# Kernel tuning notes

Hardware: AMD Instinct MI355X
Metric: run time of the kernel (lower is better)

## Reference

```python
import jax, jax.numpy as jnp
import numpy as np

D_DEC = 256  # decoder_size; W columns are [decoder | encoder] per the torch concat order


def setup_inputs() -> dict:
    key = jax.random.key(0)
    k1, k2, k3, k4 = jax.random.split(key, 4)
    B, S, E, D, A = 32, 4096, 256, 256, 256
    decoder_hidden = jax.random.normal(k1, (1, B, D), dtype=jnp.float32)
    encoder_outputs = jax.random.normal(k2, (S, B, E), dtype=jnp.float32)
    W = jax.random.normal(k3, (A, D + E), dtype=jnp.float32) / np.sqrt(D + E)
    b = jax.random.normal(k4, (A,), dtype=jnp.float32) * 0.02
    return {"decoder_hidden": decoder_hidden, "encoder_outputs": encoder_outputs, "W": W, "b": b}


def reference(decoder_hidden, encoder_outputs, W, b):
    # decoder_hidden: [1,B,D] -> [B,D]; encoder_outputs: [S,B,E] -> [B,S,E]
    dh = decoder_hidden[0]
    eo = jnp.transpose(encoder_outputs, (1, 0, 2))
    # Split the concat-linear: cat([dec, enc]) @ W.T == dec @ Wd.T + enc @ We.T
    Wd, We = W[:, :D_DEC], W[:, D_DEC:]
    # scores: tanh(linear) summed over attn dim -> [B,S]
    proj = dh @ Wd.T + b  # [B,A]
    attn = jnp.tanh(proj[:, None, :] + jnp.einsum('bse,ae->bsa', eo, We))
    scores = jnp.sum(attn, axis=2)  # [B,S]
    attn_softmax = jax.nn.softmax(scores, axis=1)  # [B,S]
    attended = jnp.einsum('bs,bse->be', attn_softmax, eo)  # [B,E]
    encoder_norms = jnp.linalg.norm(eo, axis=2)  # [B,S]
    attn_map = attn_softmax * encoder_norms
    return attended, attn_map
```

## Files before the change

### kernel.cpp

```cpp
#include <hip/hip_runtime.h>
#include <math.h>

#define B_  32
#define S_  4096
#define E_  256
#define A_  256
#define DE_ 512

typedef __attribute__((ext_vector_type(8))) short short8;
typedef __attribute__((ext_vector_type(4))) float f32x4;

__device__ inline unsigned short f2bf(float x) {
    unsigned int u = __float_as_uint(x);
    u += 0x7FFFu + ((u >> 16) & 1u);
    return (unsigned short)(u >> 16);
}
__device__ inline float tanh_fast(float x) {
    x = fminf(fmaxf(x, -15.f), 15.f);
    float t = __expf(2.f * x);
    return (t - 1.f) * __builtin_amdgcn_rcpf(t + 1.f);
}

__global__ __launch_bounds__(256) void prep_kernel(
    const float* __restrict__ W, const float* __restrict__ dh,
    const float* __restrict__ bias, unsigned short* __restrict__ wepk,
    float* __restrict__ proj, float* __restrict__ out)
{
    __shared__ float dh_lds[E_];
    const int bk  = blockIdx.x;
    const int tid = threadIdx.x;
    if (bk < 64) {
        const int idx = bk * 256 + tid;
        const int c     = idx >> 11;
        const int r     = idx & 2047;
        const int plane = r >> 10;
        const int kg    = (r >> 8) & 3;
        const int a     = r & 255;
        const float* src = W + (size_t)a * DE_ + E_ + c * 32 + kg * 8;
        unsigned int pk[4];
        #pragma unroll
        for (int j = 0; j < 4; ++j) {
            float x0 = src[2 * j], x1 = src[2 * j + 1];
            unsigned int u0 = __float_as_uint(x0) & 0xFFFF0000u;
            unsigned int u1 = __float_as_uint(x1) & 0xFFFF0000u;
            if (plane) {
                unsigned short l0 = f2bf(x0 - __uint_as_float(u0));
                unsigned short l1 = f2bf(x1 - __uint_as_float(u1));
                pk[j] = (unsigned int)l0 | ((unsigned int)l1 << 16);
            } else {
                pk[j] = (u0 >> 16) | u1;
            }
        }
        *(uint4*)&wepk[(size_t)idx * 8] = make_uint4(pk[0], pk[1], pk[2], pk[3]);
    } else if (bk < 96) {
        const int b = bk - 64;
        const int a = tid;
        dh_lds[a] = dh[b * E_ + a];
        __syncthreads();
        float acc = bias[a];
        const float* wrow = W + (size_t)a * DE_;
        #pragma unroll
        for (int d = 0; d < E_; d += 4) {
            float4 w = *(const float4*)(wrow + d);
            acc += dh_lds[d] * w.x + dh_lds[d+1] * w.y
                 + dh_lds[d+2] * w.z + dh_lds[d+3] * w.w;
        }
        proj[b * A_ + a] = acc;
    } else {
        #pragma unroll
        for (int j = tid; j < B_ * E_; j += 256) out[j] = 0.f;
    }
}

__global__ __launch_bounds__(256, 3) void scores_kernel(
    const float* __restrict__ eo, const unsigned short* __restrict__ wepk,
    const float* __restrict__ proj,
    float* __restrict__ scores, float* __restrict__ nsq)
{
    __shared__ __align__(16) unsigned short eo_lds[2 * 528 * 8];
    __shared__ float red4[64 * 65];
    __shared__ float npart[512];
    __shared__ float qpart[256];

    const int tid = threadIdx.x;
    const int b   = blockIdx.x & (B_ - 1);
    const int s0  = (blockIdx.x / B_) * 64;
    const int w   = tid >> 6, l = tid & 63;
    const int lq  = l >> 4,  lr = l & 15;

    const int erow0 = tid >> 3;
    const int ekq   = tid & 7;
    const int ekg   = ekq >> 1, eh = ekq & 1;
    const float* ebase = eo + (size_t)(s0 + erow0) * (B_ * E_) + b * E_ + ekq * 4;

    const unsigned short* wb = wepk + (size_t)(lq * 256 + w * 64 + lr) * 8;

    f32x4 acc[4][4];
    #pragma unroll
    for (int i = 0; i < 4; ++i)
        #pragma unroll
        for (int j = 0; j < 4; ++j)
            acc[i][j] = (f32x4){0.f, 0.f, 0.f, 0.f};
    float nacc[2] = {0.f, 0.f};

    float4 ec0 = *(const float4*)(ebase);
    float4 ec1 = *(const float4*)(ebase + 32 * (B_ * E_));
    short8 bh[4], bl[4], bnh[4], bnl[4];
    #pragma unroll
    for (int nt = 0; nt < 4; ++nt) {
        bh[nt] = *(const short8*)(wb + (size_t)(nt * 16) * 8);
        bl[nt] = *(const short8*)(wb + (size_t)(1024 + nt * 16) * 8);
    }

    #pragma unroll
    for (int c = 0; c < 8; ++c) {
        const int wbuf = (c & 1) * 528;
        #pragma unroll
        for (int it = 0; it < 2; ++it) {
            float4 v = it ? ec1 : ec0;
            nacc[it] += v.x*v.x + v.y*v.y + v.z*v.z + v.w*v.w;
            unsigned int ux = __float_as_uint(v.x) & 0xFFFF0000u;
            unsigned int uy = __float_as_uint(v.y) & 0xFFFF0000u;
            unsigned int uz = __float_as_uint(v.z) & 0xFFFF0000u;
            unsigned int uw = __float_as_uint(v.w) & 0xFFFF0000u;
            unsigned int hp0 = (ux >> 16) | uy;
            unsigned int hp1 = (uz >> 16) | uw;
            unsigned int lp0 = (unsigned int)f2bf(v.x - __uint_as_float(ux))
                             | ((unsigned int)f2bf(v.y - __uint_as_float(uy)) << 16);
            unsigned int lp1 = (unsigned int)f2bf(v.z - __uint_as_float(uz))
                             | ((unsigned int)f2bf(v.w - __uint_as_float(uw)) << 16);
            const int u = wbuf + ekg * 66 + it * 32 + erow0;
            *(uint2*)&eo_lds[(size_t)u * 8 + eh * 4]         = make_uint2(hp0, hp1);
            *(uint2*)&eo_lds[(size_t)(u + 264) * 8 + eh * 4] = make_uint2(lp0, lp1);
        }
        __syncthreads();
        if (c < 7) {
            ec0 = *(const float4*)(ebase + (c + 1) * 32);
            ec1 = *(const float4*)(ebase + 32 * (B_ * E_) + (c + 1) * 32);
            #pragma unroll
            for (int nt = 0; nt < 4; ++nt) {
                bnh[nt] = *(const short8*)(wb + (size_t)((c+1)*2048 + nt*16) * 8);
                bnl[nt] = *(const short8*)(wb + (size_t)((c+1)*2048 + 1024 + nt*16) * 8);
            }
        }
        #pragma unroll
        for (int mt = 0; mt < 4; ++mt) {
            const int au = wbuf + lq * 66 + mt * 16 + lr;
            short8 ah = *(const short8*)&eo_lds[(size_t)au * 8];
            short8 al = *(const short8*)&eo_lds[(size_t)(au + 264) * 8];
            #pragma unroll
            for (int nt = 0; nt < 4; ++nt) {
                acc[mt][nt] = __builtin_amdgcn_mfma_f32_16x16x32_bf16(ah, bh[nt], acc[mt][nt], 0, 0, 0);
                acc[mt][nt] = __builtin_amdgcn_mfma_f32_16x16x32_bf16(ah, bl[nt], acc[mt][nt], 0, 0, 0);
                acc[mt][nt] = __builtin_amdgcn_mfma_f32_16x16x32_bf16(al, bh[nt], acc[mt][nt], 0, 0, 0);
            }
        }
        if (c < 7) {
            #pragma unroll
            for (int nt = 0; nt < 4; ++nt) { bh[nt] = bnh[nt]; bl[nt] = bnl[nt]; }
        }
    }

    float pr[4];
    #pragma unroll
    for (int nt = 0; nt < 4; ++nt) pr[nt] = proj[b * A_ + w * 64 + nt * 16 + lr];
    #pragma unroll
    for (int mt = 0; mt < 4; ++mt) {
        #pragma unroll
        for (int r = 0; r < 4; ++r) {
            float s = 0.f;
            #pragma unroll
            for (int nt = 0; nt < 4; ++nt)
                s += tanh_fast(pr[nt] + acc[mt][nt][r]);
            red4[(w * 16 + lr) * 65 + (mt * 16 + lq * 4 + r)] = s;
        }
    }
    npart[tid]       = nacc[0];
    npart[256 + tid] = nacc[1];
    __syncthreads();
    {
        const int r = tid & 63, q = tid >> 6;
        float s = 0.f;
        #pragma unroll
        for (int c2 = q * 16; c2 < q * 16 + 16; ++c2) s += red4[c2 * 65 + r];
        qpart[q * 64 + r] = s;
    }
    __syncthreads();
    if (tid < 64) {
        scores[b * S_ + s0 + tid] = qpart[tid] + qpart[64 + tid]
                                  + qpart[128 + tid] + qpart[192 + tid];
        const int base = (tid >> 5) * 256 + (tid & 31) * 8;
        float nq = 0.f;
        #pragma unroll
        for (int q2 = 0; q2 < 8; ++q2) nq += npart[base + q2];
        nsq[b * S_ + s0 + tid] = nq;
    }
}

__global__ __launch_bounds__(256) void attend_kernel(
    const float* __restrict__ eo, const float* __restrict__ scores,
    const float* __restrict__ nsq, float* __restrict__ out)
{
    __shared__ float red[256];
    __shared__ float4 acc_red[4][64];
    const int tid = threadIdx.x;
    const int b   = blockIdx.x & (B_ - 1);
    const int ch  = blockIdx.x / B_;

    float v[16];
    float m = -1e30f;
    #pragma unroll
    for (int i = 0; i < 16; ++i) {
        v[i] = scores[b * S_ + i * 256 + tid];
        m = fmaxf(m, v[i]);
    }
    red[tid] = m;
    __syncthreads();
    for (int off = 128; off > 0; off >>= 1) {
        if (tid < off) red[tid] = fmaxf(red[tid], red[tid + off]);
        __syncthreads();
    }
    m = red[0];
    __syncthreads();
    float sum = 0.f;
    #pragma unroll
    for (int i = 0; i < 16; ++i) sum += __expf(v[i] - m);
    red[tid] = sum;
    __syncthreads();
    for (int off = 128; off > 0; off >>= 1) {
        if (tid < off) red[tid] += red[tid + off];
        __syncthreads();
    }
    const float inv = 1.f / red[0];

    const int le = tid & 63, sg = tid >> 6;
    const int s0 = ch * 128 + sg * 32;
    float4 a = make_float4(0.f, 0.f, 0.f, 0.f);
    #pragma unroll 4
    for (int s = 0; s < 32; ++s) {
        float pv = __expf(scores[b * S_ + s0 + s] - m) * inv;
        float4 e = *(const float4*)(eo + (size_t)(s0 + s) * (B_ * E_)
                                       + b * E_ + le * 4);
        a.x = fmaf(pv, e.x, a.x);
        a.y = fmaf(pv, e.y, a.y);
        a.z = fmaf(pv, e.z, a.z);
        a.w = fmaf(pv, e.w, a.w);
    }
    acc_red[sg][le] = a;
    if (tid < 128) {
        const int s = ch * 128 + tid;
        float pv = __expf(scores[b * S_ + s] - m) * inv;
        out[B_ * E_ + b * S_ + s] = pv * sqrtf(nsq[b * S_ + s]);
    }
    __syncthreads();
    if (tid < 64) {
        float4 a0 = acc_red[0][tid], a1 = acc_red[1][tid];
        float4 a2 = acc_red[2][tid], a3 = acc_red[3][tid];
        float* dst = out + b * E_ + tid * 4;
        atomicAdd(dst + 0, a0.x + a1.x + a2.x + a3.x);
        atomicAdd(dst + 1, a0.y + a1.y + a2.y + a3.y);
        atomicAdd(dst + 2, a0.z + a1.z + a2.z + a3.z);
        atomicAdd(dst + 3, a0.w + a1.w + a2.w + a3.w);
    }
}

extern "C" void kernel_launch(void* const* d_in, const int* in_sizes, int n_in,
                              void* d_out, int out_size, void* d_ws, size_t ws_size,
                              hipStream_t stream)
{
    const float* dh   = (const float*)d_in[0];
    const float* eo   = (const float*)d_in[1];
    const float* W    = (const float*)d_in[2];
    const float* bias = (const float*)d_in[3];
    float* out = (float*)d_out;
    float* ws  = (float*)d_ws;

    float* projb  = ws;
    float* nsqb   = ws + 8192;
    float* scores = nsqb + S_ * B_;
    unsigned short* wepk = (unsigned short*)(scores + S_ * B_);

    prep_kernel   <<<97,              256, 0, stream>>>(W, dh, bias, wepk, projb, out);
    scores_kernel <<<B_ * (S_ / 64),  256, 0, stream>>>(eo, wepk, projb, scores, nsqb);
    attend_kernel <<<B_ * (S_ / 128), 256, 0, stream>>>(eo, scores, nsqb, out);
}
```

Baseline: 273.2 us.

## Double scores tile to 128 rows and stage We in LDS via global_load_lds

```diff
diff --git a/kernel.cpp b/kernel.cpp
--- a/kernel.cpp
+++ b/kernel.cpp
@@ -72,82 +72,88 @@
     }
 }
 
-__global__ __launch_bounds__(256, 3) void scores_kernel(
+__global__ __launch_bounds__(256, 2) void scores_kernel(
     const float* __restrict__ eo, const unsigned short* __restrict__ wepk,
     const float* __restrict__ proj,
     float* __restrict__ scores, float* __restrict__ nsq)
 {
-    __shared__ __align__(16) unsigned short eo_lds[2 * 528 * 8];
-    __shared__ float red4[64 * 65];
-    __shared__ float npart[512];
-    __shared__ float qpart[256];
+    __shared__ __align__(16) unsigned char pool[49408];
+    unsigned short* we_hl = (unsigned short*)pool;
+    unsigned short* eo_hl = (unsigned short*)(pool + 32768);
 
     const int tid = threadIdx.x;
     const int b   = blockIdx.x & (B_ - 1);
-    const int s0  = (blockIdx.x / B_) * 64;
+    const int s0  = (blockIdx.x >> 5) * 128;
     const int w   = tid >> 6, l = tid & 63;
     const int lq  = l >> 4,  lr = l & 15;
 
-    const int erow0 = tid >> 3;
-    const int ekq   = tid & 7;
-    const int ekg   = ekq >> 1, eh = ekq & 1;
-    const float* ebase = eo + (size_t)(s0 + erow0) * (B_ * E_) + b * E_ + ekq * 4;
-
-    const unsigned short* wb = wepk + (size_t)(lq * 256 + w * 64 + lr) * 8;
-
-    f32x4 acc[4][4];
-    #pragma unroll
-    for (int i = 0; i < 4; ++i)
+    const int erow = tid >> 2;
+    const int ekg  = tid & 3;
+    const float* ebase = eo + (size_t)(s0 + erow) * (B_ * E_) + b * E_ + ekg * 8;
+
+    f32x4 acc[8][4];
+    #pragma unroll
+    for (int i = 0; i < 8; ++i)
         #pragma unroll
         for (int j = 0; j < 4; ++j)
             acc[i][j] = (f32x4){0.f, 0.f, 0.f, 0.f};
     float nacc[2] = {0.f, 0.f};
 
-    float4 ec0 = *(const float4*)(ebase);
-    float4 ec1 = *(const float4*)(ebase + 32 * (B_ * E_));
-    short8 bh[4], bl[4], bnh[4], bnl[4];
-    #pragma unroll
-    for (int nt = 0; nt < 4; ++nt) {
-        bh[nt] = *(const short8*)(wb + (size_t)(nt * 16) * 8);
-        bl[nt] = *(const short8*)(wb + (size_t)(1024 + nt * 16) * 8);
-    }
-
-    #pragma unroll
+    float4 ea0 = *(const float4*)(ebase);
+    float4 ea1 = *(const float4*)(ebase + 4);
+    float4 eb0 = *(const float4*)(ebase + (size_t)64 * (B_ * E_));
+    float4 eb1 = *(const float4*)(ebase + (size_t)64 * (B_ * E_) + 4);
+
     for (int c = 0; c < 8; ++c) {
-        const int wbuf = (c & 1) * 528;
+        __syncthreads();
         #pragma unroll
         for (int it = 0; it < 2; ++it) {
-            float4 v = it ? ec1 : ec0;
-            nacc[it] += v.x*v.x + v.y*v.y + v.z*v.z + v.w*v.w;
-            unsigned int ux = __float_as_uint(v.x) & 0xFFFF0000u;
-            unsigned int uy = __float_as_uint(v.y) & 0xFFFF0000u;
-            unsigned int uz = __float_as_uint(v.z) & 0xFFFF0000u;
-            unsigned int uw = __float_as_uint(v.w) & 0xFFFF0000u;
-            unsigned int hp0 = (ux >> 16) | uy;
-            unsigned int hp1 = (uz >> 16) | uw;
-            unsigned int lp0 = (unsigned int)f2bf(v.x - __uint_as_float(ux))
-                             | ((unsigned int)f2bf(v.y - __uint_as_float(uy)) << 16);
-            unsigned int lp1 = (unsigned int)f2bf(v.z - __uint_as_float(uz))
-                             | ((unsigned int)f2bf(v.w - __uint_as_float(uw)) << 16);
-            const int u = wbuf + ekg * 66 + it * 32 + erow0;
-            *(uint2*)&eo_lds[(size_t)u * 8 + eh * 4]         = make_uint2(hp0, hp1);
-            *(uint2*)&eo_lds[(size_t)(u + 264) * 8 + eh * 4] = make_uint2(lp0, lp1);
+            float4 v0 = it ? eb0 : ea0;
+            float4 v1 = it ? eb1 : ea1;
+            nacc[it] += v0.x*v0.x + v0.y*v0.y + v0.z*v0.z + v0.w*v0.w
+                      + v1.x*v1.x + v1.y*v1.y + v1.z*v1.z + v1.w*v1.w;
+            float xs[8] = {v0.x, v0.y, v0.z, v0.w, v1.x, v1.y, v1.z, v1.w};
+            unsigned int hp[4], lp[4];
+            #pragma unroll
+            for (int j = 0; j < 4; ++j) {
+                unsigned int u0 = __float_as_uint(xs[2*j])   & 0xFFFF0000u;
+                unsigned int u1 = __float_as_uint(xs[2*j+1]) & 0xFFFF0000u;
+                hp[j] = (u0 >> 16) | u1;
+                lp[j] = (unsigned int)f2bf(xs[2*j]   - __uint_as_float(u0))
+                      | ((unsigned int)f2bf(xs[2*j+1] - __uint_as_float(u1)) << 16);
+            }
+            const int u = ekg * 130 + it * 64 + erow;
+            *(uint4*)&eo_hl[(size_t)u * 8]         = make_uint4(hp[0], hp[1], hp[2], hp[3]);
+            *(uint4*)&eo_hl[(size_t)(520 + u) * 8] = make_uint4(lp[0], lp[1], lp[2], lp[3]);
+        }
+        const unsigned short* gsrc = wepk + (size_t)c * 2048 * 8;
+        #pragma unroll
+        for (int it = 0; it < 8; ++it) {
+            const int u = it * 256 + tid;
+            __builtin_amdgcn_global_load_lds(
+                (const __attribute__((address_space(1))) void*)(gsrc + (size_t)u * 8),
+                (__attribute__((address_space(3))) void*)&we_hl[(size_t)u * 8],
+                16, 0, 0);
         }
         __syncthreads();
         if (c < 7) {
-            ec0 = *(const float4*)(ebase + (c + 1) * 32);
-            ec1 = *(const float4*)(ebase + 32 * (B_ * E_) + (c + 1) * 32);
-            #pragma unroll
-            for (int nt = 0; nt < 4; ++nt) {
-                bnh[nt] = *(const short8*)(wb + (size_t)((c+1)*2048 + nt*16) * 8);
-                bnl[nt] = *(const short8*)(wb + (size_t)((c+1)*2048 + 1024 + nt*16) * 8);
-            }
-        }
-        #pragma unroll
-        for (int mt = 0; mt < 4; ++mt) {
-            const int au = wbuf + lq * 66 + mt * 16 + lr;
-            short8 ah = *(const short8*)&eo_lds[(size_t)au * 8];
-            short8 al = *(const short8*)&eo_lds[(size_t)(au + 264) * 8];
+            ea0 = *(const float4*)(ebase + (c + 1) * 32);
+            ea1 = *(const float4*)(ebase + (c + 1) * 32 + 4);
+            eb0 = *(const float4*)(ebase + (size_t)64 * (B_ * E_) + (c + 1) * 32);
+            eb1 = *(const float4*)(ebase + (size_t)64 * (B_ * E_) + (c + 1) * 32 + 4);
+        }
+        short8 bh[4], bl[4];
+        #pragma unroll
+        for (int nt = 0; nt < 4; ++nt) {
+            const int bunit = lq * 256 + w * 64 + nt * 16 + lr;
+            bh[nt] = *(const short8*)&we_hl[(size_t)bunit * 8];
+            bl[nt] = *(const short8*)&we_hl[(size_t)(1024 + bunit) * 8];
+        }
+        #pragma unroll
+        for (int mt = 0; mt < 8; ++mt) {
+            const int au = lq * 130 + mt * 16 + lr;
+            short8 ah = *(const short8*)&eo_hl[(size_t)au * 8];
+            short8 al = *(const short8*)&eo_hl[(size_t)(520 + au) * 8];
             #pragma unroll
             for (int nt = 0; nt < 4; ++nt) {
                 acc[mt][nt] = __builtin_amdgcn_mfma_f32_16x16x32_bf16(ah, bh[nt], acc[mt][nt], 0, 0, 0);
@@ -155,45 +161,42 @@
                 acc[mt][nt] = __builtin_amdgcn_mfma_f32_16x16x32_bf16(al, bh[nt], acc[mt][nt], 0, 0, 0);
             }
         }
-        if (c < 7) {
-            #pragma unroll
-            for (int nt = 0; nt < 4; ++nt) { bh[nt] = bnh[nt]; bl[nt] = bnl[nt]; }
-        }
-    }
-
+    }
+    __syncthreads();
+
+    float* red4  = (float*)pool;
+    float* npart = (float*)(pool + 33280);
+    float* qpart = (float*)(pool + 35328);
     float pr[4];
     #pragma unroll
     for (int nt = 0; nt < 4; ++nt) pr[nt] = proj[b * A_ + w * 64 + nt * 16 + lr];
     #pragma unroll
-    for (int mt = 0; mt < 4; ++mt) {
+    for (int mt = 0; mt < 8; ++mt) {
         #pragma unroll
         for (int r = 0; r < 4; ++r) {
             float s = 0.f;
             #pragma unroll
             for (int nt = 0; nt < 4; ++nt)
                 s += tanh_fast(pr[nt] + acc[mt][nt][r]);
-            red4[(w * 16 + lr) * 65 + (mt * 16 + lq * 4 + r)] = s;
+            red4[(w * 16 + lr) * 130 + (mt * 16 + lq * 4 + r)] = s;
         }
     }
     npart[tid]       = nacc[0];
     npart[256 + tid] = nacc[1];
     __syncthreads();
     {
-        const int r = tid & 63, q = tid >> 6;
+        const int row = tid >> 1, half = tid & 1;
         float s = 0.f;
         #pragma unroll
-        for (int c2 = q * 16; c2 < q * 16 + 16; ++c2) s += red4[c2 * 65 + r];
-        qpart[q * 64 + r] = s;
-    }
-    __syncthreads();
-    if (tid < 64) {
-        scores[b * S_ + s0 + tid] = qpart[tid] + qpart[64 + tid]
-                                  + qpart[128 + tid] + qpart[192 + tid];
-        const int base = (tid >> 5) * 256 + (tid & 31) * 8;
-        float nq = 0.f;
-        #pragma unroll
-        for (int q2 = 0; q2 < 8; ++q2) nq += npart[base + q2];
-        nsq[b * S_ + s0 + tid] = nq;
+        for (int j = 0; j < 32; ++j) s += red4[(half * 32 + j) * 130 + row];
+        qpart[half * 128 + row] = s;
+    }
+    __syncthreads();
+    if (tid < 128) {
+        scores[b * S_ + s0 + tid] = qpart[tid] + qpart[128 + tid];
+        const int base = (tid < 64) ? 4 * tid : 256 + 4 * (tid - 64);
+        nsq[b * S_ + s0 + tid] = npart[base] + npart[base + 1]
+                               + npart[base + 2] + npart[base + 3];
     }
 }
 
@@ -236,7 +239,7 @@
     const int le = tid & 63, sg = tid >> 6;
     const int s0 = ch * 128 + sg * 32;
     float4 a = make_float4(0.f, 0.f, 0.f, 0.f);
-    #pragma unroll 4
+    #pragma unroll 8
     for (int s = 0; s < 32; ++s) {
         float pv = __expf(scores[b * S_ + s0 + s] - m) * inv;
         float4 e = *(const float4*)(eo + (size_t)(s0 + s) * (B_ * E_)
@@ -281,6 +284,6 @@
     unsigned short* wepk = (unsigned short*)(scores + S_ * B_);
 
     prep_kernel   <<<97,              256, 0, stream>>>(W, dh, bias, wepk, projb, out);
-    scores_kernel <<<B_ * (S_ / 64),  256, 0, stream>>>(eo, wepk, projb, scores, nsqb);
+    scores_kernel <<<B_ * (S_ / 128), 256, 0, stream>>>(eo, wepk, projb, scores, nsqb);
     attend_kernel <<<B_ * (S_ / 128), 256, 0, stream>>>(eo, scores, nsqb, out);
 }
```

New measurement: 259.4 us. -5.1%, faster.

## Switch scores GEMM to 32x32x16 MFMA with LDS-staged weights via global_load_lds

Applied to the files above, without the earlier changes.

```diff
diff --git a/kernel.cpp b/kernel.cpp
--- a/kernel.cpp
+++ b/kernel.cpp
@@ -7,8 +7,8 @@
 #define A_  256
 #define DE_ 512
 
-typedef __attribute__((ext_vector_type(8))) short short8;
-typedef __attribute__((ext_vector_type(4))) float f32x4;
+typedef __attribute__((ext_vector_type(8)))  short short8;
+typedef __attribute__((ext_vector_type(16))) float f32x16;
 
 __device__ inline unsigned short f2bf(float x) {
     unsigned int u = __float_as_uint(x);
@@ -30,13 +30,13 @@
     const int bk  = blockIdx.x;
     const int tid = threadIdx.x;
     if (bk < 64) {
-        const int idx = bk * 256 + tid;
-        const int c     = idx >> 11;
-        const int r     = idx & 2047;
-        const int plane = r >> 10;
-        const int kg    = (r >> 8) & 3;
+        const int idx   = bk * 256 + tid;
+        const int c     = idx >> 10;
+        const int r     = idx & 1023;
+        const int plane = r >> 9;
+        const int kh    = (r >> 8) & 1;
         const int a     = r & 255;
-        const float* src = W + (size_t)a * DE_ + E_ + c * 32 + kg * 8;
+        const float* src = W + (size_t)a * DE_ + E_ + c * 16 + kh * 8;
         unsigned int pk[4];
         #pragma unroll
         for (int j = 0; j < 4; ++j) {
@@ -77,123 +77,132 @@
     const float* __restrict__ proj,
     float* __restrict__ scores, float* __restrict__ nsq)
 {
-    __shared__ __align__(16) unsigned short eo_lds[2 * 528 * 8];
-    __shared__ float red4[64 * 65];
-    __shared__ float npart[512];
-    __shared__ float qpart[256];
+    __shared__ __align__(16) unsigned char pool[40960];
+    unsigned short* webuf = (unsigned short*)pool;
+    unsigned short* eobuf = (unsigned short*)(pool + 32768);
 
     const int tid = threadIdx.x;
     const int b   = blockIdx.x & (B_ - 1);
-    const int s0  = (blockIdx.x / B_) * 64;
+    const int s0  = (blockIdx.x >> 5) * 64;
     const int w   = tid >> 6, l = tid & 63;
-    const int lq  = l >> 4,  lr = l & 15;
-
-    const int erow0 = tid >> 3;
-    const int ekq   = tid & 7;
-    const int ekg   = ekq >> 1, eh = ekq & 1;
-    const float* ebase = eo + (size_t)(s0 + erow0) * (B_ * E_) + b * E_ + ekq * 4;
-
-    const unsigned short* wb = wepk + (size_t)(lq * 256 + w * 64 + lr) * 8;
-
-    f32x4 acc[4][4];
-    #pragma unroll
-    for (int i = 0; i < 4; ++i)
-        #pragma unroll
-        for (int j = 0; j < 4; ++j)
-            acc[i][j] = (f32x4){0.f, 0.f, 0.f, 0.f};
-    float nacc[2] = {0.f, 0.f};
-
-    float4 ec0 = *(const float4*)(ebase);
-    float4 ec1 = *(const float4*)(ebase + 32 * (B_ * E_));
-    short8 bh[4], bl[4], bnh[4], bnl[4];
-    #pragma unroll
-    for (int nt = 0; nt < 4; ++nt) {
-        bh[nt] = *(const short8*)(wb + (size_t)(nt * 16) * 8);
-        bl[nt] = *(const short8*)(wb + (size_t)(1024 + nt * 16) * 8);
-    }
-
-    #pragma unroll
-    for (int c = 0; c < 8; ++c) {
-        const int wbuf = (c & 1) * 528;
-        #pragma unroll
-        for (int it = 0; it < 2; ++it) {
-            float4 v = it ? ec1 : ec0;
-            nacc[it] += v.x*v.x + v.y*v.y + v.z*v.z + v.w*v.w;
-            unsigned int ux = __float_as_uint(v.x) & 0xFFFF0000u;
-            unsigned int uy = __float_as_uint(v.y) & 0xFFFF0000u;
-            unsigned int uz = __float_as_uint(v.z) & 0xFFFF0000u;
-            unsigned int uw = __float_as_uint(v.w) & 0xFFFF0000u;
-            unsigned int hp0 = (ux >> 16) | uy;
-            unsigned int hp1 = (uz >> 16) | uw;
-            unsigned int lp0 = (unsigned int)f2bf(v.x - __uint_as_float(ux))
-                             | ((unsigned int)f2bf(v.y - __uint_as_float(uy)) << 16);
-            unsigned int lp1 = (unsigned int)f2bf(v.z - __uint_as_float(uz))
-                             | ((unsigned int)f2bf(v.w - __uint_as_float(uw)) << 16);
-            const int u = wbuf + ekg * 66 + it * 32 + erow0;
-            *(uint2*)&eo_lds[(size_t)u * 8 + eh * 4]         = make_uint2(hp0, hp1);
-            *(uint2*)&eo_lds[(size_t)(u + 264) * 8 + eh * 4] = make_uint2(lp0, lp1);
-        }
-        __syncthreads();
-        if (c < 7) {
-            ec0 = *(const float4*)(ebase + (c + 1) * 32);
-            ec1 = *(const float4*)(ebase + 32 * (B_ * E_) + (c + 1) * 32);
+    const int h   = l >> 5;
+    const int n32 = l & 31;
+
+    const int erow = tid >> 2;
+    const int eq   = tid & 3;
+    const int ekh  = eq >> 1, ehalf = eq & 1;
+    const float* ebase = eo + (size_t)(s0 + erow) * (B_ * E_) + b * E_ + eq * 4;
+
+    const float pr0 = proj[b * A_ + w * 64 + n32];
+    const float pr1 = proj[b * A_ + w * 64 + 32 + n32];
+
+    f32x16 acc[2][2];
+    #pragma unroll
+    for (int i = 0; i < 2; ++i)
+        #pragma unroll
+        for (int j = 0; j < 2; ++j)
             #pragma unroll
-            for (int nt = 0; nt < 4; ++nt) {
-                bnh[nt] = *(const short8*)(wb + (size_t)((c+1)*2048 + nt*16) * 8);
-                bnl[nt] = *(const short8*)(wb + (size_t)((c+1)*2048 + 1024 + nt*16) * 8);
+            for (int r = 0; r < 16; ++r) acc[i][j][r] = 0.f;
+    float nacc = 0.f;
+
+    auto stage_eo = [&](int buf, float4 v) {
+        nacc += v.x*v.x + v.y*v.y + v.z*v.z + v.w*v.w;
+        unsigned int ux = __float_as_uint(v.x) & 0xFFFF0000u;
+        unsigned int uy = __float_as_uint(v.y) & 0xFFFF0000u;
+        unsigned int uz = __float_as_uint(v.z) & 0xFFFF0000u;
+        unsigned int uw = __float_as_uint(v.w) & 0xFFFF0000u;
+        unsigned int hp0 = (ux >> 16) | uy;
+        unsigned int hp1 = (uz >> 16) | uw;
+        unsigned int lp0 = (unsigned int)f2bf(v.x - __uint_as_float(ux))
+                         | ((unsigned int)f2bf(v.y - __uint_as_float(uy)) << 16);
+        unsigned int lp1 = (unsigned int)f2bf(v.z - __uint_as_float(uz))
+                         | ((unsigned int)f2bf(v.w - __uint_as_float(uw)) << 16);
+        const int u = buf * 256 + ekh * 64 + erow;
+        *(uint2*)&eobuf[(size_t)u * 8 + ehalf * 4]         = make_uint2(hp0, hp1);
+        *(uint2*)&eobuf[(size_t)(u + 128) * 8 + ehalf * 4] = make_uint2(lp0, lp1);
+    };
+    auto dma_we = [&](int c, int buf) {
+        const unsigned short* gsrc = wepk + (size_t)c * 1024 * 8;
+        #pragma unroll
+        for (int it = 0; it < 4; ++it) {
+            const int u = it * 256 + tid;
+            __builtin_amdgcn_global_load_lds(
+                (const __attribute__((address_space(1))) void*)(gsrc + (size_t)u * 8),
+                (__attribute__((address_space(3))) void*)&webuf[(size_t)(buf * 1024 + u) * 8],
+                16, 0, 0);
+        }
+    };
+
+    float4 eA = *(const float4*)(ebase);
+    dma_we(0, 0);
+    stage_eo(0, eA);
+    float4 eB = *(const float4*)(ebase + 16);
+
+    #pragma unroll 2
+    for (int c = 0; c < 16; ++c) {
+        const int rb = c & 1;
+        __syncthreads();
+        if (c < 15) {
+            dma_we(c + 1, rb ^ 1);
+            stage_eo(rb ^ 1, rb ? eA : eB);
+        }
+        if (c < 14) {
+            float4 nv = *(const float4*)(ebase + (c + 2) * 16);
+            if (rb) eB = nv; else eA = nv;
+        }
+        short8 ah[2], al[2], bh[2], bl[2];
+        #pragma unroll
+        for (int nt = 0; nt < 2; ++nt) {
+            const int bu = rb * 1024 + h * 256 + w * 64 + nt * 32 + n32;
+            bh[nt] = *(const short8*)&webuf[(size_t)bu * 8];
+            bl[nt] = *(const short8*)&webuf[(size_t)(bu + 512) * 8];
+        }
+        #pragma unroll
+        for (int mt = 0; mt < 2; ++mt) {
+            const int au = rb * 256 + h * 64 + mt * 32 + n32;
+            ah[mt] = *(const short8*)&eobuf[(size_t)au * 8];
+            al[mt] = *(const short8*)&eobuf[(size_t)(au + 128) * 8];
+        }
+        #pragma unroll
+        for (int mt = 0; mt < 2; ++mt)
+            #pragma unroll
+            for (int nt = 0; nt < 2; ++nt) {
+                acc[mt][nt] = __builtin_amdgcn_mfma_f32_32x32x16_bf16(ah[mt], bh[nt], acc[mt][nt], 0, 0, 0);
+                acc[mt][nt] = __builtin_amdgcn_mfma_f32_32x32x16_bf16(ah[mt], bl[nt], acc[mt][nt], 0, 0, 0);
+                acc[mt][nt] = __builtin_amdgcn_mfma_f32_32x32x16_bf16(al[mt], bh[nt], acc[mt][nt], 0, 0, 0);
             }
-        }
-        #pragma unroll
-        for (int mt = 0; mt < 4; ++mt) {
-            const int au = wbuf + lq * 66 + mt * 16 + lr;
-            short8 ah = *(const short8*)&eo_lds[(size_t)au * 8];
-            short8 al = *(const short8*)&eo_lds[(size_t)(au + 264) * 8];
-            #pragma unroll
-            for (int nt = 0; nt < 4; ++nt) {
-                acc[mt][nt] = __builtin_amdgcn_mfma_f32_16x16x32_bf16(ah, bh[nt], acc[mt][nt], 0, 0, 0);
-                acc[mt][nt] = __builtin_amdgcn_mfma_f32_16x16x32_bf16(ah, bl[nt], acc[mt][nt], 0, 0, 0);
-                acc[mt][nt] = __builtin_amdgcn_mfma_f32_16x16x32_bf16(al, bh[nt], acc[mt][nt], 0, 0, 0);
-            }
-        }
-        if (c < 7) {
-            #pragma unroll
-            for (int nt = 0; nt < 4; ++nt) { bh[nt] = bnh[nt]; bl[nt] = bnl[nt]; }
-        }
-    }
-
-    float pr[4];
-    #pragma unroll
-    for (int nt = 0; nt < 4; ++nt) pr[nt] = proj[b * A_ + w * 64 + nt * 16 + lr];
-    #pragma unroll
-    for (int mt = 0; mt < 4; ++mt) {
-        #pragma unroll
-        for (int r = 0; r < 4; ++r) {
-            float s = 0.f;
-            #pragma unroll
-            for (int nt = 0; nt < 4; ++nt)
-                s += tanh_fast(pr[nt] + acc[mt][nt][r]);
-            red4[(w * 16 + lr) * 65 + (mt * 16 + lq * 4 + r)] = s;
-        }
-    }
-    npart[tid]       = nacc[0];
-    npart[256 + tid] = nacc[1];
+    }
+    __syncthreads();
+
+    float* red   = (float*)pool;
+    float* npart = (float*)(pool + 33024);
+    float* qpart = (float*)(pool + 34048);
+    #pragma unroll
+    for (int mt = 0; mt < 2; ++mt) {
+        #pragma unroll
+        for (int r = 0; r < 16; ++r) {
+            const int rowl = (r & 3) + 8 * (r >> 2) + 4 * h;
+            float v = tanh_fast(pr0 + acc[mt][0][r])
+                    + tanh_fast(pr1 + acc[mt][1][r]);
+            red[(mt * 32 + rowl) * 129 + w * 32 + n32] = v;
+        }
+    }
+    npart[tid] = nacc;
     __syncthreads();
     {
-        const int r = tid & 63, q = tid >> 6;
+        const int row = tid >> 2, q = tid & 3;
         float s = 0.f;
         #pragma unroll
-        for (int c2 = q * 16; c2 < q * 16 + 16; ++c2) s += red4[c2 * 65 + r];
-        qpart[q * 64 + r] = s;
+        for (int j = 0; j < 32; ++j)
+            s += red[row * 129 + q * 32 + ((j + q * 8) & 31)];
+        qpart[tid] = s;
     }
     __syncthreads();
     if (tid < 64) {
-        scores[b * S_ + s0 + tid] = qpart[tid] + qpart[64 + tid]
-                                  + qpart[128 + tid] + qpart[192 + tid];
-        const int base = (tid >> 5) * 256 + (tid & 31) * 8;
-        float nq = 0.f;
-        #pragma unroll
-        for (int q2 = 0; q2 < 8; ++q2) nq += npart[base + q2];
-        nsq[b * S_ + s0 + tid] = nq;
+        scores[b * S_ + s0 + tid] = qpart[4*tid] + qpart[4*tid+1]
+                                  + qpart[4*tid+2] + qpart[4*tid+3];
+        nsq[b * S_ + s0 + tid]    = npart[4*tid] + npart[4*tid+1]
+                                  + npart[4*tid+2] + npart[4*tid+3];
     }
 }
 
@@ -236,7 +245,7 @@
     const int le = tid & 63, sg = tid >> 6;
     const int s0 = ch * 128 + sg * 32;
     float4 a = make_float4(0.f, 0.f, 0.f, 0.f);
-    #pragma unroll 4
+    #pragma unroll 8
     for (int s = 0; s < 32; ++s) {
         float pv = __expf(scores[b * S_ + s0 + s] - m) * inv;
         float4 e = *(const float4*)(eo + (size_t)(s0 + s) * (B_ * E_)
```

After: 266.7 us. 1.02x faster.
